# Performance work log

Hardware: AMD Instinct MI355X
Metric: run time of the kernel (lower is better)

## Reference

```python
import jax, jax.numpy as jnp
import numpy as np

# ---- static config (model_cfg equivalents) ----
H_GRIDS, W_GRIDS = 2, 2
S_TOKENS = 1024          # H*W with H=W=32
C_DIM = 768
NUM_HEADS = 12
D_HEAD = 64
TOKEN_SIZE = (24, 24)    # model_cfg.token_size
SCALE = 1.0
BETA = 1.2               # model_cfg.beta (token_norm path)
GAMMA = 3.0              # model_cfg.gamma
CUTTING_HP = 0.1         # model_cfg.cutting_hp
TEMPERATURE = 0.07       # model_cfg.temperature
N_CLUSTERS = 32


def _l2norm(x, eps=1e-12):
    # matches torch F.normalize(dim=-1)
    n = jnp.linalg.norm(x, axis=-1, keepdims=True)
    return x / jnp.maximum(n, eps)


def setup_inputs() -> dict:
    key = jax.random.key(0)
    k1, k2, k3 = jax.random.split(key, 3)
    B = H_GRIDS * W_GRIDS
    ex = jax.random.normal(k1, (H_GRIDS, W_GRIDS, S_TOKENS, C_DIM), jnp.float32)
    indices = jax.random.randint(k2, (B * S_TOKENS,), 0, N_CLUSTERS)
    v_ext = jax.random.normal(k3, (B * NUM_HEADS, TOKEN_SIZE[0], TOKEN_SIZE[1], D_HEAD), jnp.float32)
    return {"ex_feats_grid": ex, "v_ext": v_ext, "indices": indices}


def _forward(ex_feats_grid, v_ext, indices):
    hg, wg, S, C = ex_feats_grid.shape
    B = hg * wg
    H = W = int(S ** 0.5)
    N = B * S
    x = ex_feats_grid.reshape(N, C)                          # [N, C]
    nh = v_ext.shape[0] // B
    Dh = v_ext.shape[-1]

    # --- value branch: bilinear resize (align_corners=False) to (H, W) ---
    v = v_ext.transpose(0, 3, 1, 2)                          # [B*nh, Dh, t0, t1]
    v = jax.image.resize(v, (B * nh, Dh, H, W), method='bilinear')
    v = v.reshape(B, nh, Dh, S).transpose(1, 0, 3, 2).reshape(nh, N, Dh)  # [nh, N, Dh]

    # --- proxy candidate mask: same cluster label OR 8-neighbor within same grid block ---
    indices_mask = indices[:, None] == indices[None, :]       # [N, N]
    rr, cc = jnp.meshgrid(jnp.arange(H), jnp.arange(W), indexing='ij')
    coords = jnp.stack([rr.ravel(), cc.ravel()], axis=1)      # [S, 2]
    delta = coords[:, None, :] - coords[None, :, :]           # [S, S, 2]
    window = (jnp.max(jnp.abs(delta), axis=-1) <= 1) & (jnp.sum(jnp.abs(delta), axis=-1) > 0)
    blk = jnp.arange(N) // S
    neighbor = (blk[:, None] == blk[None, :]) & jnp.tile(window, (B, B))  # block_diag(window x B)
    cand = indices_mask | neighbor                            # [N, N]

    count = jnp.maximum(cand.sum(-1, keepdims=True), 1).astype(x.dtype)
    proxy = (cand.astype(x.dtype) @ x) / count                # [N, C] averaged proxy feats

    key_feats = _l2norm(x)
    attn = _l2norm(proxy) @ key_feats.T                       # [N, N] proxy similarity (mini_iters=0)
    attn = attn.reshape(B, S, N) * SCALE

    # --- token_norm rescale (static beta/gamma) ---
    sim_mean = jnp.maximum(attn.mean(-1, keepdims=True), 0.0)  # sim_mean[sim_mean<0]=0
    attn = (attn - sim_mean * BETA) * GAMMA

    # --- dynamic threshold cut + masked softmax ---
    cut = jnp.minimum(attn.max(-1, keepdims=True), CUTTING_HP)
    attn = jnp.where(attn < cut, -jnp.inf, attn)
    attn = jax.nn.softmax(attn / TEMPERATURE, axis=-1)        # each row keeps >=1 finite entry

    out = jnp.einsum('bsn,hnd->hsbd', attn, v)                # [nh, S, B, Dh]
    return out.transpose(1, 2, 0, 3).reshape(S, B, nh * Dh)   # [S, B, nh*Dh]


def reference(ex_feats_grid, v_ext, indices):
    return _forward(ex_feats_grid, v_ext, indices)
```

## Files before the change

### kernel.cpp

```cpp
#include <hip/hip_runtime.h>
#include <hip/hip_bf16.h>
#include <stdint.h>

typedef __attribute__((ext_vector_type(8))) short    bf16x8;
typedef __attribute__((ext_vector_type(4))) float    f32x4;
typedef __attribute__((ext_vector_type(8))) unsigned short u16x8;
typedef __attribute__((ext_vector_type(4))) unsigned short u16x4;
typedef __attribute__((ext_vector_type(8))) _Float16 f16x8;

#define N_TOK   4096
#define C_DIM   768
#define NCLU    32
#define ZSPLIT  8

__device__ __forceinline__ uint16_t f2bf(float f){
  union { float f; unsigned u; } v; v.f = f;
  unsigned r = v.u + 0x7fffu + ((v.u >> 16) & 1u);
  return (uint16_t)(r >> 16);
}

__device__ __forceinline__ void gl2lds16(const void* g, void* l){
  __builtin_amdgcn_global_load_lds(
      (const __attribute__((address_space(1))) unsigned int*)g,
      (__attribute__((address_space(3))) unsigned int*)l, 16, 0, 0);
}

__global__ __launch_bounds__(256) void csum_part_k(const float* __restrict__ x, const int* __restrict__ idx,
                                                   float* __restrict__ csum){
  __shared__ float lacc[NCLU * 256];
  __shared__ int   sidx[32];
  const int tc = blockIdx.x, chunk = blockIdx.y;
  const int tid = threadIdx.x;
  #pragma unroll
  for (int u = 0; u < NCLU; ++u) lacc[u * 256 + tid] = 0.f;
  if (tid < 32) sidx[tid] = idx[tc * 32 + tid];
  __syncthreads();
  const int ch = chunk * 256 + tid;
  const float* xb = x + (size_t)(tc * 32) * C_DIM + ch;
  #pragma unroll 8
  for (int t = 0; t < 32; ++t){
    int c = sidx[t];
    lacc[c * 256 + tid] += xb[(size_t)t * C_DIM];
  }
  __syncthreads();
  float* cb = csum + chunk * 256 + tid;
  #pragma unroll
  for (int c = 0; c < NCLU; ++c) atomicAdd(cb + (size_t)c * C_DIM, lacc[c * 256 + tid]);
}

__global__ __launch_bounds__(256) void proxy_key_k(const float* __restrict__ x, const int* __restrict__ idx,
                                                   const float* __restrict__ csum,
                                                   uint16_t* __restrict__ An, uint16_t* __restrict__ Bn){
  const int i = blockIdx.x * 4 + (threadIdx.x >> 6);
  const int lane = threadIdx.x & 63;
  const int ci = idx[i];
  const int b = i >> 10, s = i & 1023, r = s >> 5, w = s & 31;
  const int drs[8] = {-1,-1,-1, 0, 0, 1, 1, 1};
  const int dws[8] = {-1, 0, 1,-1, 1,-1, 0, 1};
  int js[8]; unsigned mask = 0;
  #pragma unroll
  for (int t = 0; t < 8; ++t){
    int rr = r + drs[t], ww = w + dws[t];
    bool ok = ((unsigned)rr < 32u) && ((unsigned)ww < 32u);
    int j = (b << 10) + (rr << 5) + ww;
    js[t] = ok ? j : i;
    if (ok && idx[js[t]] != ci) mask |= (1u << t);
  }
  const float4* xr = (const float4*)(x + (size_t)i * C_DIM);
  const float4* cr = (const float4*)(csum + (size_t)ci * C_DIM);
  float4 xs[3], ps[3]; float ssx = 0.f, ssp = 0.f;
  #pragma unroll
  for (int u = 0; u < 3; ++u){
    int c4 = u * 64 + lane;
    float4 xv = xr[c4];
    float4 pv = cr[c4];
    #pragma unroll
    for (int t = 0; t < 8; ++t)
      if (mask & (1u << t)){
        float4 nv = ((const float4*)(x + (size_t)js[t] * C_DIM))[c4];
        pv.x += nv.x; pv.y += nv.y; pv.z += nv.z; pv.w += nv.w;
      }
    xs[u] = xv; ps[u] = pv;
    ssx += xv.x*xv.x + xv.y*xv.y + xv.z*xv.z + xv.w*xv.w;
    ssp += pv.x*pv.x + pv.y*pv.y + pv.z*pv.z + pv.w*pv.w;
  }
  #pragma unroll
  for (int m = 32; m; m >>= 1){ ssx += __shfl_xor(ssx, m); ssp += __shfl_xor(ssp, m); }
  float rnx = 1.f / fmaxf(sqrtf(ssx), 1e-12f);
  float rnp = 1.f / fmaxf(sqrtf(ssp), 1e-12f);
  u16x4* Br = (u16x4*)(Bn + (size_t)i * C_DIM);
  u16x4* Ar = (u16x4*)(An + (size_t)i * C_DIM);
  #pragma unroll
  for (int u = 0; u < 3; ++u){
    int c4 = u * 64 + lane;
    u16x4 ob, oa;
    ob[0] = f2bf(xs[u].x * rnx); ob[1] = f2bf(xs[u].y * rnx);
    ob[2] = f2bf(xs[u].z * rnx); ob[3] = f2bf(xs[u].w * rnx);
    oa[0] = f2bf(ps[u].x * rnp); oa[1] = f2bf(ps[u].y * rnp);
    oa[2] = f2bf(ps[u].z * rnp); oa[3] = f2bf(ps[u].w * rnp);
    Br[c4] = ob;
    Ar[c4] = oa;
  }
}

template<int MODE>
__global__ __launch_bounds__(256) void gemm_bt_k(const uint16_t* __restrict__ A, const uint16_t* __restrict__ B,
                                                 int ldA, int ldB, int K,
                                                 _Float16* __restrict__ Sout,
                                                 const float* __restrict__ rden,
                                                 _Float16* __restrict__ Obuf,
                                                 const float* __restrict__ vext,
                                                 uint16_t* __restrict__ Vt){
  __shared__ __align__(16) char smem[65536];
  const int g = blockIdx.x;
  const int tid = threadIdx.x;

  if (MODE == 0 && g >= 1024){
    float* ld = (float*)smem;
    const int rb = g - 1024, bh = rb >> 5, y = rb & 31;
    const int b = bh / 12, h = bh % 12;
    const float* base = vext + (size_t)bh * 576 * 64;
    float sy = (y + 0.5f) * 0.75f - 0.5f;
    float fy0 = floorf(sy); float fy = sy - fy0; int y0 = (int)fy0;
    int iy0 = y0 < 0 ? 0 : y0;  int iy1 = (y0 + 1 > 23) ? 23 : y0 + 1;
    const int d = tid & 63, xg = tid >> 6;
    #pragma unroll
    for (int jj = 0; jj < 8; ++jj){
      int xx = xg + 4 * jj;
      float sx = (xx + 0.5f) * 0.75f - 0.5f;
      float fx0 = floorf(sx); float fx = sx - fx0; int x0 = (int)fx0;
      int ix0 = x0 < 0 ? 0 : x0;  int ix1 = (x0 + 1 > 23) ? 23 : x0 + 1;
      float v00 = base[(iy0 * 24 + ix0) * 64 + d];
      float v01 = base[(iy0 * 24 + ix1) * 64 + d];
      float v10 = base[(iy1 * 24 + ix0) * 64 + d];
      float v11 = base[(iy1 * 24 + ix1) * 64 + d];
      ld[d * 33 + xx] = (1.f - fy) * ((1.f - fx) * v00 + fx * v01)
                      +        fy  * ((1.f - fx) * v10 + fx * v11);
    }
    __syncthreads();
    const int xx = tid & 31, dg = tid >> 5;
    const int n = b * 1024 + y * 32 + xx;
    #pragma unroll
    for (int jj = 0; jj < 8; ++jj){
      int d2 = dg * 8 + jj;
      Vt[(size_t)(h * 64 + d2) * 4096 + n] = f2bf(ld[d2 * 33 + xx]);
    }
    return;
  }

  const int lane = tid & 63, wid = tid >> 6;
  const int q = lane >> 4, l16 = lane & 15;
  const int wrow = wid & 1, wcol = wid >> 1;

  const int xcd = g & 7;
  const int j   = g >> 3;
  int i0, n0, kt0, per, z = 0;
  const int KT = K >> 6;
  if (MODE == 0){
    int sq = j >> 4;
    int mi = ((sq >> 2) << 2) + ((j >> 2) & 3);
    int ni = ((sq & 3) << 2) + (j & 3);
    i0 = (((xcd >> 1) << 3) + mi) * 128;
    n0 = (((xcd & 1) << 4) + ni) * 128;
    kt0 = 0; per = KT;
  } else {
    z  = xcd;
    i0 = (j / 6) * 128;
    n0 = (j % 6) * 128;
    per = KT >> 3; kt0 = z * per;
  }

  f32x4 acc[4][4] = {};

  auto STAGE = [&](int c, int kt){
    const int k0 = kt << 6;
    char* sb = smem + c * 32768;
    #pragma unroll
    for (int t = 0; t < 4; ++t){
      int p   = t * 256 + tid;
      int row = p >> 3, kc = p & 7;
      int kcs = kc ^ (row & 7);
      gl2lds16(A + (size_t)(i0 + row) * ldA + k0 + kcs * 8, sb + p * 16);
      gl2lds16(B + (size_t)(n0 + row) * ldB + k0 + kcs * 8, sb + 16384 + p * 16);
    }
  };

  STAGE(0, kt0);
  asm volatile("s_waitcnt vmcnt(0)" ::: "memory");
  __builtin_amdgcn_s_barrier();

  int cur = 0;
  const int ktEnd = kt0 + per;
  for (int kt = kt0; kt < ktEnd; ++kt){
    if (kt + 1 < ktEnd) STAGE(cur ^ 1, kt + 1);
    const char* sb = smem + cur * 32768;
    #pragma unroll
    for (int ks = 0; ks < 2; ++ks){
      bf16x8 af[4], bfr[4];
      #pragma unroll
      for (int mt = 0; mt < 4; ++mt){
        int row = wrow * 64 + mt * 16 + l16;
        int ck  = (ks * 4 + q) ^ (row & 7);
        af[mt] = *(const bf16x8*)(sb + row * 128 + ck * 16);
      }
      #pragma unroll
      for (int nt = 0; nt < 4; ++nt){
        int row = wcol * 64 + nt * 16 + l16;
        int ck  = (ks * 4 + q) ^ (row & 7);
        bfr[nt] = *(const bf16x8*)(sb + 16384 + row * 128 + ck * 16);
      }
      #pragma unroll
      for (int mt = 0; mt < 4; ++mt)
        #pragma unroll
        for (int nt = 0; nt < 4; ++nt)
          acc[mt][nt] = __builtin_amdgcn_mfma_f32_16x16x32_bf16(af[mt], bfr[nt], acc[mt][nt], 0, 0, 0);
    }
    asm volatile("s_waitcnt vmcnt(0)" ::: "memory");
    __builtin_amdgcn_s_barrier();
    cur ^= 1;
  }

  _Float16* Pz = (MODE == 1) ? (Obuf + (size_t)z * N_TOK * C_DIM) : nullptr;
  #pragma unroll
  for (int mt = 0; mt < 4; ++mt){
    #pragma unroll
    for (int r = 0; r < 4; ++r){
      int row = i0 + wrow * 64 + mt * 16 + q * 4 + r;
      float rd = (MODE == 1) ? rden[row] : 0.f;
      #pragma unroll
      for (int nt = 0; nt < 4; ++nt){
        int col = n0 + wcol * 64 + nt * 16 + l16;
        float v = acc[mt][nt][r];
        if (MODE == 0)
          Sout[(size_t)row * 4096 + col] = (_Float16)v;
        else
          Pz[(size_t)row * C_DIM + col] = (_Float16)(v * rd);
      }
    }
  }
}

__global__ __launch_bounds__(256) void rowsoftmax_k(const _Float16* __restrict__ S, uint16_t* __restrict__ P,
                                                    float* __restrict__ rden){
  const int row = blockIdx.x * 4 + (threadIdx.x >> 6);
  const int lane = threadIdx.x & 63;
  const f16x8* Sr = (const f16x8*)(S + (size_t)row * 4096);
  f16x8 h[8];
  #pragma unroll
  for (int c = 0; c < 8; ++c) h[c] = Sr[c * 64 + lane];
  float v[64];
  float mx = -3.4e38f, sm = 0.f;
  #pragma unroll
  for (int c = 0; c < 8; ++c)
    #pragma unroll
    for (int e = 0; e < 8; ++e){
      float f = (float)h[c][e];
      v[c * 8 + e] = f; mx = fmaxf(mx, f); sm += f;
    }
  #pragma unroll
  for (int m = 32; m; m >>= 1){ mx = fmaxf(mx, __shfl_xor(mx, m)); sm += __shfl_xor(sm, m); }

  float bmu  = 1.2f * fmaxf(sm * (1.f / 4096.f), 0.f);
  float amax = 3.0f * (mx - bmu);
  float cut  = fminf(amax, 0.1f);

  float den = 0.f;
  u16x8 o[8];
  #pragma unroll
  for (int c = 0; c < 8; ++c)
    #pragma unroll
    for (int e = 0; e < 8; ++e){
      float a  = 3.0f * (v[c * 8 + e] - bmu);
      float ev = (a >= cut) ? __expf((a - amax) * (1.f / 0.07f)) : 0.f;
      den += ev;
      o[c][e] = f2bf(ev);
    }
  #pragma unroll
  for (int m = 32; m; m >>= 1) den += __shfl_xor(den, m);
  if (lane == 0) rden[row] = 1.f / den;

  u16x8* Pr = (u16x8*)(P + (size_t)row * 4096);
  #pragma unroll
  for (int c = 0; c < 8; ++c) Pr[c * 64 + lane] = o[c];
}

__global__ __launch_bounds__(256) void reduce_k(const _Float16* __restrict__ Pz, float* __restrict__ out){
  const int t = blockIdx.x * 256 + threadIdx.x;
  const int row = t / 96, c8 = t % 96;
  const size_t base = (size_t)row * C_DIM + c8 * 8;
  const size_t zs = (size_t)N_TOK * C_DIM;
  float o[8] = {0.f, 0.f, 0.f, 0.f, 0.f, 0.f, 0.f, 0.f};
  #pragma unroll
  for (int z = 0; z < ZSPLIT; ++z){
    f16x8 a = *(const f16x8*)(Pz + base + (size_t)z * zs);
    #pragma unroll
    for (int e = 0; e < 8; ++e) o[e] += (float)a[e];
  }
  const int s = row & 1023, bb = row >> 10;
  float* dst = out + (size_t)s * 3072 + bb * 768 + c8 * 8;
  ((float4*)dst)[0] = make_float4(o[0], o[1], o[2], o[3]);
  ((float4*)dst)[1] = make_float4(o[4], o[5], o[6], o[7]);
}

extern "C" void kernel_launch(void* const* d_in, const int* in_sizes, int n_in,
                              void* d_out, int out_size, void* d_ws, size_t ws_size,
                              hipStream_t stream){
  (void)in_sizes; (void)n_in; (void)out_size; (void)ws_size;
  const float* ex   = (const float*)d_in[0];
  const float* vext = (const float*)d_in[1];
  const int*   idx  = (const int*)d_in[2];
  float* out = (float*)d_out;
  char* ws = (char*)d_ws;

  uint16_t* P    = (uint16_t*)(ws);
  uint16_t* Vt   = (uint16_t*)(ws + 33554432);
  char*     R    = ws + 39845888;
  uint16_t* An   = (uint16_t*)(R);
  uint16_t* Bn   = (uint16_t*)(R + 6291456);
  _Float16* S16  = (_Float16*)(R + 12582912);
  _Float16* Pz   = (_Float16*)(R);
  float*    csum = (float*)(ws + 90177536);
  float*    rden = (float*)(ws + 90275840);

  hipMemsetAsync(csum, 0, NCLU * C_DIM * sizeof(float), stream);
  csum_part_k<<<dim3(128, 3), 256, 0, stream>>>(ex, idx, csum);
  proxy_key_k<<<1024, 256, 0, stream>>>(ex, idx, csum, An, Bn);
  gemm_bt_k<0><<<2560, 256, 0, stream>>>(An, Bn, 768, 768, 768, S16, nullptr, nullptr, vext, Vt);
  rowsoftmax_k<<<1024, 256, 0, stream>>>(S16, P, rden);
  gemm_bt_k<1><<<1536, 256, 0, stream>>>(P, Vt, 4096, 4096, 4096, nullptr, rden, Pz, nullptr, nullptr);
  reduce_k<<<1536, 256, 0, stream>>>(Pz, out);
}
```

Measured before the change: 183.4 us.

## Fuse split-K reduction into GEMM epilogue via atomics; move V resize to proxy kernel

The split-K P·V GEMM now atomically adds its scaled fp32 partials straight into the zeroed output, replacing the fp16 partial buffer and the separate reduce kernel. The bilinear V resize and transpose blocks move from the score GEMM launch into the proxy/key normalization kernel, so the score GEMM launches only its tile blocks. This removes one launch and the write and read of eight partial output slabs, at the cost of a memset of the output and contended float atomics. Summation order becomes nondeterministic.

New measurement: 238.1 us. 1.3x slower.

```diff
diff --git a/kernel.cpp b/kernel.cpp
--- a/kernel.cpp
+++ b/kernel.cpp
@@ -11,7 +11,6 @@
 #define N_TOK   4096
 #define C_DIM   768
 #define NCLU    32
-#define ZSPLIT  8
 
 __device__ __forceinline__ uint16_t f2bf(float f){
   union { float f; unsigned u; } v; v.f = f;
@@ -50,74 +49,14 @@
 
 __global__ __launch_bounds__(256) void proxy_key_k(const float* __restrict__ x, const int* __restrict__ idx,
                                                    const float* __restrict__ csum,
-                                                   uint16_t* __restrict__ An, uint16_t* __restrict__ Bn){
-  const int i = blockIdx.x * 4 + (threadIdx.x >> 6);
-  const int lane = threadIdx.x & 63;
-  const int ci = idx[i];
-  const int b = i >> 10, s = i & 1023, r = s >> 5, w = s & 31;
-  const int drs[8] = {-1,-1,-1, 0, 0, 1, 1, 1};
-  const int dws[8] = {-1, 0, 1,-1, 1,-1, 0, 1};
-  int js[8]; unsigned mask = 0;
-  #pragma unroll
-  for (int t = 0; t < 8; ++t){
-    int rr = r + drs[t], ww = w + dws[t];
-    bool ok = ((unsigned)rr < 32u) && ((unsigned)ww < 32u);
-    int j = (b << 10) + (rr << 5) + ww;
-    js[t] = ok ? j : i;
-    if (ok && idx[js[t]] != ci) mask |= (1u << t);
-  }
-  const float4* xr = (const float4*)(x + (size_t)i * C_DIM);
-  const float4* cr = (const float4*)(csum + (size_t)ci * C_DIM);
-  float4 xs[3], ps[3]; float ssx = 0.f, ssp = 0.f;
-  #pragma unroll
-  for (int u = 0; u < 3; ++u){
-    int c4 = u * 64 + lane;
-    float4 xv = xr[c4];
-    float4 pv = cr[c4];
-    #pragma unroll
-    for (int t = 0; t < 8; ++t)
-      if (mask & (1u << t)){
-        float4 nv = ((const float4*)(x + (size_t)js[t] * C_DIM))[c4];
-        pv.x += nv.x; pv.y += nv.y; pv.z += nv.z; pv.w += nv.w;
-      }
-    xs[u] = xv; ps[u] = pv;
-    ssx += xv.x*xv.x + xv.y*xv.y + xv.z*xv.z + xv.w*xv.w;
-    ssp += pv.x*pv.x + pv.y*pv.y + pv.z*pv.z + pv.w*pv.w;
-  }
-  #pragma unroll
-  for (int m = 32; m; m >>= 1){ ssx += __shfl_xor(ssx, m); ssp += __shfl_xor(ssp, m); }
-  float rnx = 1.f / fmaxf(sqrtf(ssx), 1e-12f);
-  float rnp = 1.f / fmaxf(sqrtf(ssp), 1e-12f);
-  u16x4* Br = (u16x4*)(Bn + (size_t)i * C_DIM);
-  u16x4* Ar = (u16x4*)(An + (size_t)i * C_DIM);
-  #pragma unroll
-  for (int u = 0; u < 3; ++u){
-    int c4 = u * 64 + lane;
-    u16x4 ob, oa;
-    ob[0] = f2bf(xs[u].x * rnx); ob[1] = f2bf(xs[u].y * rnx);
-    ob[2] = f2bf(xs[u].z * rnx); ob[3] = f2bf(xs[u].w * rnx);
-    oa[0] = f2bf(ps[u].x * rnp); oa[1] = f2bf(ps[u].y * rnp);
-    oa[2] = f2bf(ps[u].z * rnp); oa[3] = f2bf(ps[u].w * rnp);
-    Br[c4] = ob;
-    Ar[c4] = oa;
-  }
-}
-
-template<int MODE>
-__global__ __launch_bounds__(256) void gemm_bt_k(const uint16_t* __restrict__ A, const uint16_t* __restrict__ B,
-                                                 int ldA, int ldB, int K,
-                                                 _Float16* __restrict__ Sout,
-                                                 const float* __restrict__ rden,
-                                                 _Float16* __restrict__ Obuf,
-                                                 const float* __restrict__ vext,
-                                                 uint16_t* __restrict__ Vt){
-  __shared__ __align__(16) char smem[65536];
-  const int g = blockIdx.x;
+                                                   uint16_t* __restrict__ An, uint16_t* __restrict__ Bn,
+                                                   const float* __restrict__ vext,
+                                                   uint16_t* __restrict__ Vt){
+  __shared__ float ld[64 * 33];
   const int tid = threadIdx.x;
 
-  if (MODE == 0 && g >= 1024){
-    float* ld = (float*)smem;
-    const int rb = g - 1024, bh = rb >> 5, y = rb & 31;
+  if (blockIdx.x >= 1024){
+    const int rb = (int)blockIdx.x - 1024, bh = rb >> 5, y = rb & 31;
     const int b = bh / 12, h = bh % 12;
     const float* base = vext + (size_t)bh * 576 * 64;
     float sy = (y + 0.5f) * 0.75f - 0.5f;
@@ -147,6 +86,68 @@
     }
     return;
   }
+
+  const int i = blockIdx.x * 4 + (tid >> 6);
+  const int lane = tid & 63;
+  const int ci = idx[i];
+  const int b = i >> 10, s = i & 1023, r = s >> 5, w = s & 31;
+  const int drs[8] = {-1,-1,-1, 0, 0, 1, 1, 1};
+  const int dws[8] = {-1, 0, 1,-1, 1,-1, 0, 1};
+  int js[8]; unsigned mask = 0;
+  #pragma unroll
+  for (int t = 0; t < 8; ++t){
+    int rr = r + drs[t], ww = w + dws[t];
+    bool ok = ((unsigned)rr < 32u) && ((unsigned)ww < 32u);
+    int j = (b << 10) + (rr << 5) + ww;
+    js[t] = ok ? j : i;
+    if (ok && idx[js[t]] != ci) mask |= (1u << t);
+  }
+  const float4* xr = (const float4*)(x + (size_t)i * C_DIM);
+  const float4* cr = (const float4*)(csum + (size_t)ci * C_DIM);
+  float4 xs[3], ps[3]; float ssx = 0.f, ssp = 0.f;
+  #pragma unroll
+  for (int u = 0; u < 3; ++u){
+    int c4 = u * 64 + lane;
+    float4 xv = xr[c4];
+    float4 pv = cr[c4];
+    #pragma unroll
+    for (int t = 0; t < 8; ++t)
+      if (mask & (1u << t)){
+        float4 nv = ((const float4*)(x + (size_t)js[t] * C_DIM))[c4];
+        pv.x += nv.x; pv.y += nv.y; pv.z += nv.z; pv.w += nv.w;
+      }
+    xs[u] = xv; ps[u] = pv;
+    ssx += xv.x*xv.x + xv.y*xv.y + xv.z*xv.z + xv.w*xv.w;
+    ssp += pv.x*pv.x + pv.y*pv.y + pv.z*pv.z + pv.w*pv.w;
+  }
+  #pragma unroll
+  for (int m = 32; m; m >>= 1){ ssx += __shfl_xor(ssx, m); ssp += __shfl_xor(ssp, m); }
+  float rnx = 1.f / fmaxf(sqrtf(ssx), 1e-12f);
+  float rnp = 1.f / fmaxf(sqrtf(ssp), 1e-12f);
+  u16x4* Br = (u16x4*)(Bn + (size_t)i * C_DIM);
+  u16x4* Ar = (u16x4*)(An + (size_t)i * C_DIM);
+  #pragma unroll
+  for (int u = 0; u < 3; ++u){
+    int c4 = u * 64 + lane;
+    u16x4 ob, oa;
+    ob[0] = f2bf(xs[u].x * rnx); ob[1] = f2bf(xs[u].y * rnx);
+    ob[2] = f2bf(xs[u].z * rnx); ob[3] = f2bf(xs[u].w * rnx);
+    oa[0] = f2bf(ps[u].x * rnp); oa[1] = f2bf(ps[u].y * rnp);
+    oa[2] = f2bf(ps[u].z * rnp); oa[3] = f2bf(ps[u].w * rnp);
+    Br[c4] = ob;
+    Ar[c4] = oa;
+  }
+}
+
+template<int MODE>
+__global__ __launch_bounds__(256) void gemm_bt_k(const uint16_t* __restrict__ A, const uint16_t* __restrict__ B,
+                                                 int ldA, int ldB, int K,
+                                                 _Float16* __restrict__ Sout,
+                                                 const float* __restrict__ rden,
+                                                 float* __restrict__ out){
+  __shared__ __align__(16) char smem[65536];
+  const int g = blockIdx.x;
+  const int tid = threadIdx.x;
 
   const int lane = tid & 63, wid = tid >> 6;
   const int q = lane >> 4, l16 = lane & 15;
@@ -220,21 +221,26 @@
     cur ^= 1;
   }
 
-  _Float16* Pz = (MODE == 1) ? (Obuf + (size_t)z * N_TOK * C_DIM) : nullptr;
   #pragma unroll
   for (int mt = 0; mt < 4; ++mt){
     #pragma unroll
     for (int r = 0; r < 4; ++r){
       int row = i0 + wrow * 64 + mt * 16 + q * 4 + r;
-      float rd = (MODE == 1) ? rden[row] : 0.f;
-      #pragma unroll
-      for (int nt = 0; nt < 4; ++nt){
-        int col = n0 + wcol * 64 + nt * 16 + l16;
-        float v = acc[mt][nt][r];
-        if (MODE == 0)
-          Sout[(size_t)row * 4096 + col] = (_Float16)v;
-        else
-          Pz[(size_t)row * C_DIM + col] = (_Float16)(v * rd);
+      if (MODE == 0){
+        #pragma unroll
+        for (int nt = 0; nt < 4; ++nt){
+          int col = n0 + wcol * 64 + nt * 16 + l16;
+          Sout[(size_t)row * 4096 + col] = (_Float16)acc[mt][nt][r];
+        }
+      } else {
+        float rd = rden[row];
+        const int s = row & 1023, bb = row >> 10;
+        float* dst = out + (size_t)s * 3072 + bb * 768;
+        #pragma unroll
+        for (int nt = 0; nt < 4; ++nt){
+          int col = n0 + wcol * 64 + nt * 16 + l16;
+          atomicAdd(dst + col, acc[mt][nt][r] * rd);
+        }
       }
     }
   }
@@ -282,24 +288,6 @@
   u16x8* Pr = (u16x8*)(P + (size_t)row * 4096);
   #pragma unroll
   for (int c = 0; c < 8; ++c) Pr[c * 64 + lane] = o[c];
-}
-
-__global__ __launch_bounds__(256) void reduce_k(const _Float16* __restrict__ Pz, float* __restrict__ out){
-  const int t = blockIdx.x * 256 + threadIdx.x;
-  const int row = t / 96, c8 = t % 96;
-  const size_t base = (size_t)row * C_DIM + c8 * 8;
-  const size_t zs = (size_t)N_TOK * C_DIM;
-  float o[8] = {0.f, 0.f, 0.f, 0.f, 0.f, 0.f, 0.f, 0.f};
-  #pragma unroll
-  for (int z = 0; z < ZSPLIT; ++z){
-    f16x8 a = *(const f16x8*)(Pz + base + (size_t)z * zs);
-    #pragma unroll
-    for (int e = 0; e < 8; ++e) o[e] += (float)a[e];
-  }
-  const int s = row & 1023, bb = row >> 10;
-  float* dst = out + (size_t)s * 3072 + bb * 768 + c8 * 8;
-  ((float4*)dst)[0] = make_float4(o[0], o[1], o[2], o[3]);
-  ((float4*)dst)[1] = make_float4(o[4], o[5], o[6], o[7]);
 }
 
 extern "C" void kernel_launch(void* const* d_in, const int* in_sizes, int n_in,
@@ -318,15 +306,14 @@
   uint16_t* An   = (uint16_t*)(R);
   uint16_t* Bn   = (uint16_t*)(R + 6291456);
   _Float16* S16  = (_Float16*)(R + 12582912);
-  _Float16* Pz   = (_Float16*)(R);
   float*    csum = (float*)(ws + 90177536);
   float*    rden = (float*)(ws + 90275840);
 
+  hipMemsetAsync(out, 0, (size_t)1024 * 4 * 768 * sizeof(float), stream);
   hipMemsetAsync(csum, 0, NCLU * C_DIM * sizeof(float), stream);
   csum_part_k<<<dim3(128, 3), 256, 0, stream>>>(ex, idx, csum);
-  proxy_key_k<<<1024, 256, 0, stream>>>(ex, idx, csum, An, Bn);
-  gemm_bt_k<0><<<2560, 256, 0, stream>>>(An, Bn, 768, 768, 768, S16, nullptr, nullptr, vext, Vt);
+  proxy_key_k<<<2560, 256, 0, stream>>>(ex, idx, csum, An, Bn, vext, Vt);
+  gemm_bt_k<0><<<1024, 256, 0, stream>>>(An, Bn, 768, 768, 768, S16, nullptr, nullptr);
   rowsoftmax_k<<<1024, 256, 0, stream>>>(S16, P, rden);
-  gemm_bt_k<1><<<1536, 256, 0, stream>>>(P, Vt, 4096, 4096, 4096, nullptr, rden, Pz, nullptr, nullptr);
-  reduce_k<<<1536, 256, 0, stream>>>(Pz, out);
-}
+  gemm_bt_k<1><<<1536, 256, 0, stream>>>(P, Vt, 4096, 4096, 4096, nullptr, rden, out);
+}
```
